# Performance work log

Hardware: AMD Instinct MI355X
Metric: run time of the kernel (lower is better)

## Reference

```python
import jax, jax.numpy as jnp
import numpy as np

N = 16384      # num_nodes (mamba seq_len)
D = 256        # input_dim
HOPS = 3
E = 262144     # num edges
DI = 512       # d_inner = expand*dim
DS = 16        # d_state
DC = 4         # d_conv


def _ln(x, g, b):
    m = jnp.mean(x, -1, keepdims=True)
    v = jnp.var(x, -1, keepdims=True)
    return (x - m) / jnp.sqrt(v + 1e-5) * g + b


def setup_inputs() -> dict:
    key = jax.random.key(0)
    ks = jax.random.split(key, 20)
    g = lambda i, shape, s=0.02: jax.random.normal(ks[i], shape, jnp.float32) * s
    z = lambda *s: jnp.zeros(s, jnp.float32)
    o = lambda *s: jnp.ones(s, jnp.float32)
    return {
        "x": jax.random.normal(ks[0], (HOPS, N, D), jnp.float32),
        "edge_index": jax.random.randint(ks[1], (2, E), 0, N),
        "perm_noise": jax.random.uniform(ks[2], (N,), jnp.float32),
        "hop_w": g(3, (HOPS * D, D)), "hop_b": z(D), "hop_ln_g": o(D), "hop_ln_b": z(D),
        "gat_w": g(4, (D, D)), "gat_att_src": g(5, (D,)), "gat_att_dst": g(6, (D,)), "gat_b": z(D),
        "in_proj_w": g(7, (D, 2 * DI)),
        "conv_w": g(8, (DI, DC), 0.1),
        "x_proj_w": g(9, (DI, DS + 1)),
        "dt_w": g(10, (1, DI)), "dt_b": z(DI),
        "A_log": g(11, (DI, DS)),
        "D_param": o(DI),
        "out_w": g(12, (DI, D)), "out_b": z(D),
        "mlp_w1": g(13, (2 * D, D)), "mlp_b1": z(D), "mlp_ln_g": o(D), "mlp_ln_b": z(D),
        "mlp_w2": g(14, (D, D)), "mlp_b2": z(D),
    }


def _forward(x, edge_index, perm_noise, hop_w, hop_b, hop_ln_g, hop_ln_b,
             gat_w, gat_att_src, gat_att_dst, gat_b, in_proj_w, conv_w,
             x_proj_w, dt_w, dt_b, A_log, D_param, out_w, out_b,
             mlp_w1, mlp_b1, mlp_ln_g, mlp_ln_b, mlp_w2, mlp_b2):
    n = x.shape[1]
    # [hops,N,D] -> [N, hops*D] -> hop_proj
    xf = jnp.transpose(x, (1, 0, 2)).reshape(n, -1)
    xf = jax.nn.silu(_ln(xf @ hop_w + hop_b, hop_ln_g, hop_ln_b))

    # --- GATConv (heads=1, add_self_loops, negative_slope=0.2, eval dropout) ---
    h = xf @ gat_w                                   # [N,D]
    sl = jnp.arange(n)
    src = jnp.concatenate([edge_index[0], sl])
    dst = jnp.concatenate([edge_index[1], sl])
    e = jax.nn.leaky_relu((h @ gat_att_src)[src] + (h @ gat_att_dst)[dst], 0.2)
    emax = jax.ops.segment_max(e, dst, num_segments=n)
    ee = jnp.exp(e - emax[dst])
    denom = jax.ops.segment_sum(ee, dst, num_segments=n)
    alpha = ee / denom[dst]
    x_mpnn = jax.ops.segment_sum(alpha[:, None] * h[src], dst, num_segments=n) + gat_b

    # --- NodeProcessor: degree-based sort with small random noise ---
    deg = jax.ops.segment_sum(jnp.ones((edge_index.shape[1],), jnp.float32),
                              edge_index[0], num_segments=n)
    sorted_idx = jnp.argsort(deg + perm_noise * 0.1)
    u0 = xf[sorted_idx][None]                        # [1,N,D]

    # --- MambaBlock ---
    xz = u0 @ in_proj_w                              # [1,N,2*DI]
    xm, zgate = jnp.split(xz, 2, axis=-1)
    # depthwise causal conv1d (pad d_conv-1 left == torch pad both + slice[:L])
    xm_t = jnp.transpose(xm, (0, 2, 1))              # [1,DI,N]
    xm_t = jax.lax.conv_general_dilated(xm_t, conv_w[:, None, :], (1,),
                                        [(DC - 1, 0)], feature_group_count=DI)
    xm = jax.nn.silu(jnp.transpose(xm_t, (0, 2, 1)))  # [1,N,DI]
    x_dbl = xm @ x_proj_w                            # [1,N,DS+1]
    dt = jax.nn.softplus(x_dbl[..., :1] @ dt_w + dt_b)  # [1,N,DI]
    Bm = x_dbl[..., 1:]                              # [1,N,DS]
    A = -jnp.exp(A_log)                              # [DI,DS]

    def step(hst, inp):
        dti, Bi = inp                                # [1,DI],[1,DS]
        hst = jnp.exp(A * dti[..., None]) * hst + dti[..., None] * Bi[:, None, :]
        return hst, jnp.einsum('bdn,bn->bd', hst, Bi)

    h0 = jnp.zeros((1, DI, DS), xm.dtype)
    _, ys = jax.lax.scan(step, h0, (jnp.transpose(dt, (1, 0, 2)),
                                    jnp.transpose(Bm, (1, 0, 2))))
    y = jnp.transpose(ys, (1, 0, 2)) + xm * D_param  # [1,N,DI]
    y = y * jax.nn.silu(zgate)
    x_mamba = (y @ out_w + out_b)[0]                 # [N,D]

    reverse_idx = jnp.argsort(sorted_idx)
    x_mamba = x_mamba[reverse_idx]

    cat = jnp.concatenate([x_mpnn, x_mamba], axis=-1)
    out = jax.nn.silu(_ln(cat @ mlp_w1 + mlp_b1, mlp_ln_g, mlp_ln_b)) @ mlp_w2 + mlp_b2
    return out  # dim_proj is Identity (input_dim == output_dim)


def reference(x, edge_index, perm_noise, hop_w, hop_b, hop_ln_g, hop_ln_b,
              gat_w, gat_att_src, gat_att_dst, gat_b, in_proj_w, conv_w,
              x_proj_w, dt_w, dt_b, A_log, D_param, out_w, out_b,
              mlp_w1, mlp_b1, mlp_ln_g, mlp_ln_b, mlp_w2, mlp_b2):
    return _forward(x, edge_index, perm_noise, hop_w, hop_b, hop_ln_g, hop_ln_b,
                    gat_w, gat_att_src, gat_att_dst, gat_b, in_proj_w, conv_w,
                    x_proj_w, dt_w, dt_b, A_log, D_param, out_w, out_b,
                    mlp_w1, mlp_b1, mlp_ln_g, mlp_ln_b, mlp_w2, mlp_b2)
```

## Files before the change

### kernel.cpp

```cpp
#include <hip/hip_runtime.h>

#define N_   16384
#define D_   256
#define E_   262144
#define ET_  278528
#define DI_  512
#define CH_  512
#define CL_  32
#define GS_  16
#define NG_  32

typedef __attribute__((ext_vector_type(8))) short short8;
typedef __attribute__((ext_vector_type(4))) float f32x4;
typedef unsigned short ushort_t;

static __device__ __forceinline__ float wave_sum(float v){
#pragma unroll
  for (int m = 1; m < 64; m <<= 1) v += __shfl_xor(v, m);
  return v;
}
static __device__ __forceinline__ float wave_max(float v){
#pragma unroll
  for (int m = 1; m < 64; m <<= 1) v = fmaxf(v, __shfl_xor(v, m));
  return v;
}
static __device__ __forceinline__ float silu_f(float x){ return x / (1.f + __expf(-x)); }
static __device__ __forceinline__ float softplus_f(float v){
  return fmaxf(v, 0.f) + __logf(1.f + __expf(-fabsf(v)));
}
static __device__ __forceinline__ float fexp2(float x){ return __builtin_amdgcn_exp2f(x); }
static __device__ __forceinline__ ushort_t f2b(float f){
  unsigned u = __float_as_uint(f);
  return (ushort_t)((u + 0x7fffu + ((u >> 16) & 1u)) >> 16);
}
static __device__ __forceinline__ float b2f(ushort_t u){
  return __uint_as_float(((unsigned)u) << 16);
}
#define GLDS16(gp, lp) __builtin_amdgcn_global_load_lds( \
    (const __attribute__((address_space(1))) unsigned int*)(gp), \
    (__attribute__((address_space(3))) unsigned int*)(lp), 16, 0, 0)

__global__ __launch_bounds__(256) void marker_kernel(float* __restrict__ out){
  out[threadIdx.x] = 1e9f;
}

__global__ __launch_bounds__(256) void permute_kernel(const float* __restrict__ x, ushort_t* __restrict__ xcat){
  int idx = blockIdx.x * 256 + threadIdx.x;
  if (idx >= 3 * N_ * 64) return;
  int d4  = idx & 63;
  int n   = (idx >> 6) & (N_ - 1);
  int hop = idx >> 20;
  float4 v = ((const float4*)x)[((size_t)hop << 20) + ((size_t)n << 6) + d4];
  ushort4 o; o.x = f2b(v.x); o.y = f2b(v.y); o.z = f2b(v.z); o.w = f2b(v.w);
  ((ushort4*)xcat)[(size_t)n * 192 + hop * 64 + d4] = o;
}

__global__ __launch_bounds__(256) void wconv_kernel(const float* __restrict__ W, int K, int N,
                                                    ushort_t* __restrict__ BT){
  __shared__ float t[32][33];
  const int k0 = blockIdx.x * 32, n0 = blockIdx.y * 32;
  const int tr = threadIdx.x & 31, tc = threadIdx.x >> 5;
#pragma unroll
  for (int r = tc; r < 32; r += 8) {
    int k = k0 + r, n = n0 + tr;
    t[r][tr] = (k < K && n < N) ? W[(size_t)k * N + n] : 0.f;
  }
  __syncthreads();
#pragma unroll
  for (int r = tc; r < 32; r += 8) {
    int n = n0 + r, k = k0 + tr;
    BT[(size_t)n * K + k] = f2b(t[tr][r]);
  }
}

__global__ __launch_bounds__(256) void mgemm_kernel(
    const ushort_t* __restrict__ A, int lda,
    const ushort_t* __restrict__ BT, int ldbt, int N,
    void* __restrict__ C, int ldc, int c_off, int c_bf16,
    const float* __restrict__ bias, const int* __restrict__ row_map, int K)
{
  __shared__ __align__(16) ushort_t Al[64 * 32];
  __shared__ __align__(16) ushort_t Bl[64 * 32];
  const int tid = threadIdx.x;
  const int lane = tid & 63;
  const int wid = tid >> 6;
  const int wr = wid >> 1, wc = wid & 1;
  const int m0 = blockIdx.x * 64, n0 = blockIdx.y * 64;
  const int fr = lane & 15, fq = lane >> 4;
  const int srow = tid >> 2, scg = (tid & 3) << 3;
  f32x4 acc[2][2] = {};
  for (int k0 = 0; k0 < K; k0 += 32) {
    __syncthreads();
    GLDS16(&A [(size_t)(m0 + srow) * lda  + k0 + scg], &Al[(size_t)wid * 512]);
    GLDS16(&BT[(size_t)(n0 + srow) * ldbt + k0 + scg], &Bl[(size_t)wid * 512]);
    __syncthreads();
    short8 af[2], bfr[2];
#pragma unroll
    for (int m = 0; m < 2; ++m) af[m]  = *(const short8*)&Al[(wr * 32 + m * 16 + fr) * 32 + fq * 8];
#pragma unroll
    for (int n = 0; n < 2; ++n) bfr[n] = *(const short8*)&Bl[(wc * 32 + n * 16 + fr) * 32 + fq * 8];
#pragma unroll
    for (int n = 0; n < 2; ++n)
#pragma unroll
      for (int m = 0; m < 2; ++m)
        acc[m][n] = __builtin_amdgcn_mfma_f32_16x16x32_bf16(af[m], bfr[n], acc[m][n], 0, 0, 0);
  }
#pragma unroll
  for (int m = 0; m < 2; ++m)
#pragma unroll
    for (int n = 0; n < 2; ++n) {
      int col = n0 + wc * 32 + n * 16 + fr;
      if (col >= N) continue;
      float bv = bias ? bias[col] : 0.f;
#pragma unroll
      for (int j = 0; j < 4; ++j) {
        int row = m0 + wr * 32 + m * 16 + fq * 4 + j;
        int orow = row_map ? row_map[row] : row;
        float v = acc[m][n][j] + bv;
        if (c_bf16) ((ushort_t*)C)[(size_t)orow * ldc + c_off + col] = f2b(v);
        else        ((float*)C)   [(size_t)orow * ldc + c_off + col] = v;
      }
    }
}

__global__ __launch_bounds__(256) void ln_silu_kernel(const float* __restrict__ x, ushort_t* __restrict__ o8,
                                                      const float* __restrict__ g, const float* __restrict__ b){
  __shared__ float red[4];
  const int row = blockIdx.x; const int t = threadIdx.x;
  float v = x[(size_t)row * 256 + t];
  float sv = wave_sum(v);
  if ((t & 63) == 0) red[t >> 6] = sv;
  __syncthreads();
  float mean = (red[0] + red[1] + red[2] + red[3]) * (1.f / 256.f);
  __syncthreads();
  float dv = v - mean;
  float sq = wave_sum(dv * dv);
  if ((t & 63) == 0) red[t >> 6] = sq;
  __syncthreads();
  float var = (red[0] + red[1] + red[2] + red[3]) * (1.f / 256.f);
  float o = dv * rsqrtf(var + 1e-5f) * g[t] + b[t];
  o8[(size_t)row * 256 + t] = f2b(silu_f(o));
}

__global__ __launch_bounds__(256) void att_scores_kernel(const ushort_t* __restrict__ h, const float* __restrict__ asr,
                                                         const float* __restrict__ adt, float* __restrict__ as_, float* __restrict__ ad_){
  int wid = threadIdx.x >> 6, lane = threadIdx.x & 63;
  int n = blockIdx.x * 4 + wid;
  float s1 = 0.f, s2 = 0.f;
  for (int f = lane; f < 256; f += 64) {
    float hv = b2f(h[(size_t)n * 256 + f]);
    s1 = fmaf(hv, asr[f], s1); s2 = fmaf(hv, adt[f], s2);
  }
  s1 = wave_sum(s1); s2 = wave_sum(s2);
  if (lane == 0) { as_[n] = s1; ad_[n] = s2; }
}

__global__ __launch_bounds__(256) void count_kernel(const int* __restrict__ ei, int* __restrict__ cnt_in, int* __restrict__ deg_out){
  int i = blockIdx.x * 256 + threadIdx.x;
  if (i >= ET_) return;
  int dst = (i < E_) ? ei[E_ + i] : (i - E_);
  atomicAdd(&cnt_in[dst], 1);
  if (i < E_) atomicAdd(&deg_out[ei[i]], 1);
}

__global__ __launch_bounds__(1024) void scan_offsets_kernel(const int* __restrict__ cnt, int* __restrict__ off, int* __restrict__ cursor){
  __shared__ int part[1024];
  int t = threadIdx.x;
  int base = t * 16;
  int local[16]; int s = 0;
#pragma unroll
  for (int i = 0; i < 16; ++i) { local[i] = s; s += cnt[base + i]; }
  part[t] = s; __syncthreads();
  for (int d = 1; d < 1024; d <<= 1) {
    int val = part[t];
    int add = (t >= d) ? part[t - d] : 0;
    __syncthreads();
    part[t] = val + add;
    __syncthreads();
  }
  int prev = (t > 0) ? part[t - 1] : 0;
#pragma unroll
  for (int i = 0; i < 16; ++i) { int o = prev + local[i]; off[base + i] = o; cursor[base + i] = o; }
  if (t == 1023) off[N_] = part[1023];
}

__global__ __launch_bounds__(256) void scatter_kernel(const int* __restrict__ ei, int* __restrict__ cursor, int* __restrict__ csr){
  int i = blockIdx.x * 256 + threadIdx.x;
  if (i >= ET_) return;
  int dst = (i < E_) ? ei[E_ + i] : (i - E_);
  int pos = atomicAdd(&cursor[dst], 1);
  csr[pos] = i;
}

__global__ __launch_bounds__(256) void gat_agg_kernel(const int* __restrict__ ei, const int* __restrict__ off, const int* __restrict__ csr,
                                                      const float* __restrict__ as_, const float* __restrict__ ad_,
                                                      const ushort_t* __restrict__ h, const float* __restrict__ gat_b, ushort_t* __restrict__ cat){
  const int dst = blockIdx.x;
  const int t = threadIdx.x;
  const int o0 = off[dst];
  int deg = off[dst + 1] - o0;
  if (deg > 1024) deg = 1024;
  __shared__ int   ssrc[1024];
  __shared__ float se[1024];
  __shared__ float red[4];
  const float adv = ad_[dst];
  float m = -1e30f;
  for (int j = t; j < deg; j += 256) {
    int eid = csr[o0 + j];
    int src = (eid < E_) ? ei[eid] : (eid - E_);
    float e = as_[src] + adv;
    e = (e >= 0.f) ? e : 0.2f * e;
    ssrc[j] = src; se[j] = e;
    m = fmaxf(m, e);
  }
  m = wave_max(m);
  if ((t & 63) == 0) red[t >> 6] = m;
  __syncthreads();
  m = fmaxf(fmaxf(red[0], red[1]), fmaxf(red[2], red[3]));
  __syncthreads();
  float dsum = 0.f;
  for (int j = t; j < deg; j += 256) { float x = __expf(se[j] - m); se[j] = x; dsum += x; }
  dsum = wave_sum(dsum);
  if ((t & 63) == 0) red[t >> 6] = dsum;
  __syncthreads();
  float inv = 1.f / (red[0] + red[1] + red[2] + red[3]);
  float acc = gat_b[t];
  for (int j = 0; j < deg; ++j) acc = fmaf(se[j] * inv, b2f(h[(size_t)ssrc[j] * 256 + t]), acc);
  cat[(size_t)dst * 512 + t] = f2b(acc);
}

__global__ __launch_bounds__(256) void key_kernel(const int* __restrict__ degO, const float* __restrict__ noise, unsigned long long* __restrict__ keys){
  int n = blockIdx.x * 256 + threadIdx.x;
  if (n >= N_) return;
  float k = __fadd_rn((float)degO[n], __fmul_rn(noise[n], 0.1f));
  unsigned u = __float_as_uint(k);
  u = (u & 0x80000000u) ? ~u : (u | 0x80000000u);
  keys[n] = ((unsigned long long)u << 32) | (unsigned)n;
}

__global__ __launch_bounds__(256) void rank_part_kernel(const unsigned long long* __restrict__ keys, int* __restrict__ rank){
  __shared__ unsigned long long tile[512];
  const int i = blockIdx.x * 256 + threadIdx.x;
  const unsigned long long ki = keys[i];
  const int base = blockIdx.y * 512;
  for (int j = threadIdx.x; j < 512; j += 256) tile[j] = keys[base + j];
  __syncthreads();
  int r = 0;
#pragma unroll 16
  for (int j = 0; j < 512; ++j) r += (tile[j] < ki);
  atomicAdd(&rank[i], r);
}
__global__ __launch_bounds__(256) void rank_scatter_kernel(const int* __restrict__ rank, int* __restrict__ sidx){
  int i = blockIdx.x * 256 + threadIdx.x;
  sidx[rank[i]] = i;
}

__global__ __launch_bounds__(64) void gather_kernel(const ushort_t* __restrict__ xf, const int* __restrict__ sidx, ushort_t* __restrict__ u0){
  int i = blockIdx.x, t = threadIdx.x;
  ((uint2*)u0)[(size_t)i * 64 + t] = ((const uint2*)xf)[(size_t)sidx[i] * 64 + t];
}

__global__ __launch_bounds__(256) void conv_silu_kernel(const float* __restrict__ xz, const float* __restrict__ cw, ushort_t* __restrict__ xm){
  int idx = blockIdx.x * 256 + threadIdx.x;
  if (idx >= N_ * DI_) return;
  int n = idx >> 9, c = idx & 511;
  float acc = 0.f;
#pragma unroll
  for (int k = 0; k < 4; ++k) {
    int nn = n - 3 + k;
    if (nn >= 0) acc = fmaf(xz[(size_t)nn * 1024 + c], cw[c * 4 + k], acc);
  }
  xm[idx] = f2b(silu_f(acc));
}

__global__ __launch_bounds__(256) void scan_p1_kernel(const float* __restrict__ xdbl,
    const float* __restrict__ dt_w, const float* __restrict__ dt_b, const float* __restrict__ A_log,
    float* __restrict__ a_sum, float* __restrict__ b_final)
{
  const int t = threadIdx.x;
  const int d = blockIdx.x * 128 + (t >> 1);
  const int sh = (t & 1) * 8;
  const int c = blockIdx.y;
  float Ac2[8];
#pragma unroll
  for (int k = 0; k < 8; ++k) Ac2[k] = -__expf(A_log[d * 16 + sh + k]) * 1.44269504f;
  const float dwv = dt_w[d], dbv = dt_b[d];
  __shared__ float sx[CL_];
  __shared__ __align__(16) float sB[CL_][16];
  for (int idx = t; idx < CL_ * 17; idx += 256) {
    float v = xdbl[(size_t)c * (CL_ * 17) + idx];
    int row = idx / 17, col = idx - row * 17;
    if (col == 0) sx[row] = v; else sB[row][col - 1] = v;
  }
  __syncthreads();
  float h[8] = {};
  float dts = 0.f;
#pragma unroll 2
  for (int i = 0; i < CL_; ++i) {
    float dtv = softplus_f(fmaf(sx[i], dwv, dbv));
    dts += dtv;
    float4 b0 = *(const float4*)&sB[i][sh];
    float4 b1 = *(const float4*)&sB[i][sh + 4];
    h[0] = fmaf(fexp2(Ac2[0] * dtv), h[0], dtv * b0.x);
    h[1] = fmaf(fexp2(Ac2[1] * dtv), h[1], dtv * b0.y);
    h[2] = fmaf(fexp2(Ac2[2] * dtv), h[2], dtv * b0.z);
    h[3] = fmaf(fexp2(Ac2[3] * dtv), h[3], dtv * b0.w);
    h[4] = fmaf(fexp2(Ac2[4] * dtv), h[4], dtv * b1.x);
    h[5] = fmaf(fexp2(Ac2[5] * dtv), h[5], dtv * b1.y);
    h[6] = fmaf(fexp2(Ac2[6] * dtv), h[6], dtv * b1.z);
    h[7] = fmaf(fexp2(Ac2[7] * dtv), h[7], dtv * b1.w);
  }
  if ((t & 1) == 0) a_sum[c * 512 + d] = dts;
#pragma unroll
  for (int k = 0; k < 8; ++k) b_final[((size_t)c * 16 + sh + k) * 512 + d] = h[k];
}

__global__ __launch_bounds__(256) void scan_mid1_kernel(const float* __restrict__ a_sum,
    const float* __restrict__ b_final, const float* __restrict__ A_log,
    float* __restrict__ ga, float* __restrict__ gb)
{
  const int tid = blockIdx.x * 256 + threadIdx.x;
  const int d = tid & 511;
  const int s = (tid >> 9) & 15;
  const int g = tid >> 13;
  const float Ac = -__expf(A_log[d * 16 + s]);
  const int c0 = g * GS_;
  float ag = 0.f, Bg = 0.f;
  float an = a_sum[c0 * 512 + d];
  float bn = b_final[((size_t)c0 * 16 + s) * 512 + d];
#pragma unroll
  for (int k = 0; k < GS_; ++k) {
    float a = an, b = bn;
    if (k + 1 < GS_) {
      an = a_sum[(c0 + k + 1) * 512 + d];
      bn = b_final[((size_t)(c0 + k + 1) * 16 + s) * 512 + d];
    }
    Bg = fmaf(__expf(Ac * a), Bg, b);
    ag += a;
  }
  gb[((size_t)g * 16 + s) * 512 + d] = Bg;
  if (s == 0) ga[g * 512 + d] = ag;
}

__global__ __launch_bounds__(256) void scan_mid2_kernel(const float* __restrict__ ga,
    const float* __restrict__ gb, const float* __restrict__ A_log, float* __restrict__ ginit)
{
  const int tid = blockIdx.x * 256 + threadIdx.x;
  const int d = tid & 511;
  const int s = tid >> 9;
  const float Ac = -__expf(A_log[d * 16 + s]);
  float gar[NG_], gbr[NG_];
#pragma unroll
  for (int g = 0; g < NG_; ++g) {
    gar[g] = ga[g * 512 + d];
    gbr[g] = gb[((size_t)g * 16 + s) * 512 + d];
  }
  float h = 0.f;
#pragma unroll
  for (int g = 0; g < NG_; ++g) {
    ginit[((size_t)g * 16 + s) * 512 + d] = h;
    h = fmaf(__expf(Ac * gar[g]), h, gbr[g]);
  }
}

__global__ __launch_bounds__(256) void scan_mid3_kernel(const float* __restrict__ a_sum,
    const float* __restrict__ b_final, const float* __restrict__ A_log,
    const float* __restrict__ ginit, float* __restrict__ init)
{
  const int tid = blockIdx.x * 256 + threadIdx.x;
  const int d = tid & 511;
  const int s = (tid >> 9) & 15;
  const int g = tid >> 13;
  const float Ac = -__expf(A_log[d * 16 + s]);
  const int c0 = g * GS_;
  float h = ginit[((size_t)g * 16 + s) * 512 + d];
  float an = a_sum[c0 * 512 + d];
  float bn = b_final[((size_t)c0 * 16 + s) * 512 + d];
#pragma unroll
  for (int k = 0; k < GS_; ++k) {
    float a = an, b = bn;
    if (k + 1 < GS_) {
      an = a_sum[(c0 + k + 1) * 512 + d];
      bn = b_final[((size_t)(c0 + k + 1) * 16 + s) * 512 + d];
    }
    init[((size_t)(c0 + k) * 16 + s) * 512 + d] = h;
    h = fmaf(__expf(Ac * a), h, b);
  }
}

__global__ __launch_bounds__(256) void scan_p3_kernel(const float* __restrict__ xdbl,
    const float* __restrict__ dt_w, const float* __restrict__ dt_b, const float* __restrict__ A_log,
    const float* __restrict__ init, const ushort_t* __restrict__ xm, const float* __restrict__ Dp,
    const float* __restrict__ xz, ushort_t* __restrict__ y_bf)
{
  const int t = threadIdx.x;
  const int d = blockIdx.x * 128 + (t >> 1);
  const int sh = (t & 1) * 8;
  const int c = blockIdx.y;
  float Ac2[8];
#pragma unroll
  for (int k = 0; k < 8; ++k) Ac2[k] = -__expf(A_log[d * 16 + sh + k]) * 1.44269504f;
  const float dwv = dt_w[d], dbv = dt_b[d], dpv = Dp[d];
  __shared__ float sx[CL_];
  __shared__ __align__(16) float sB[CL_][16];
  for (int idx = t; idx < CL_ * 17; idx += 256) {
    float v = xdbl[(size_t)c * (CL_ * 17) + idx];
    int row = idx / 17, col = idx - row * 17;
    if (col == 0) sx[row] = v; else sB[row][col - 1] = v;
  }
  __syncthreads();
  float h[8];
#pragma unroll
  for (int k = 0; k < 8; ++k) h[k] = init[((size_t)c * 16 + sh + k) * 512 + d];
  const int n0 = c * CL_;
  const ushort_t* xmp = xm   + (size_t)n0 * 512  + d;
  const float*    zp  = xz   + (size_t)n0 * 1024 + 512 + d;
  ushort_t*       yp  = y_bf + (size_t)n0 * 512  + d;
#pragma unroll 2
  for (int i = 0; i < CL_; ++i) {
    float dtv = softplus_f(fmaf(sx[i], dwv, dbv));
    float4 b0 = *(const float4*)&sB[i][sh];
    float4 b1 = *(const float4*)&sB[i][sh + 4];
    h[0] = fmaf(fexp2(Ac2[0] * dtv), h[0], dtv * b0.x);
    h[1] = fmaf(fexp2(Ac2[1] * dtv), h[1], dtv * b0.y);
    h[2] = fmaf(fexp2(Ac2[2] * dtv), h[2], dtv * b0.z);
    h[3] = fmaf(fexp2(Ac2[3] * dtv), h[3], dtv * b0.w);
    h[4] = fmaf(fexp2(Ac2[4] * dtv), h[4], dtv * b1.x);
    h[5] = fmaf(fexp2(Ac2[5] * dtv), h[5], dtv * b1.y);
    h[6] = fmaf(fexp2(Ac2[6] * dtv), h[6], dtv * b1.z);
    h[7] = fmaf(fexp2(Ac2[7] * dtv), h[7], dtv * b1.w);
    float y = h[0] * b0.x;
    y = fmaf(h[1], b0.y, y); y = fmaf(h[2], b0.z, y); y = fmaf(h[3], b0.w, y);
    y = fmaf(h[4], b1.x, y); y = fmaf(h[5], b1.y, y); y = fmaf(h[6], b1.z, y);
    y = fmaf(h[7], b1.w, y);
    y += __shfl_xor(y, 1);
    if ((t & 1) == 0) {
      float yv = fmaf(b2f(*xmp), dpv, y);
      float z = *zp;
      *yp = f2b(yv * silu_f(z));
    }
    xmp += 512; zp += 1024; yp += 512;
  }
}

extern "C" void kernel_launch(void* const* d_in, const int* in_sizes, int n_in,
                              void* d_out, int out_size, void* d_ws, size_t ws_size,
                              hipStream_t stream)
{
  (void)in_sizes; (void)n_in; (void)out_size;
  const float* x         = (const float*)d_in[0];
  const int*   ei        = (const int*)d_in[1];
  const float* pnoise    = (const float*)d_in[2];
  const float* hop_w     = (const float*)d_in[3];
  const float* hop_b     = (const float*)d_in[4];
  const float* hop_ln_g  = (const float*)d_in[5];
  const float* hop_ln_b  = (const float*)d_in[6];
  const float* gat_w     = (const float*)d_in[7];
  const float* att_src   = (const float*)d_in[8];
  const float* att_dst   = (const float*)d_in[9];
  const float* gat_b     = (const float*)d_in[10];
  const float* in_proj_w = (const float*)d_in[11];
  const float* conv_w    = (const float*)d_in[12];
  const float* x_proj_w  = (const float*)d_in[13];
  const float* dt_w      = (const float*)d_in[14];
  const float* dt_b      = (const float*)d_in[15];
  const float* A_log     = (const float*)d_in[16];
  const float* D_param   = (const float*)d_in[17];
  const float* out_w     = (const float*)d_in[18];
  const float* out_b     = (const float*)d_in[19];
  const float* mlp_w1    = (const float*)d_in[20];
  const float* mlp_b1    = (const float*)d_in[21];
  const float* mlp_ln_g  = (const float*)d_in[22];
  const float* mlp_ln_b  = (const float*)d_in[23];
  const float* mlp_w2    = (const float*)d_in[24];
  const float* mlp_b2    = (const float*)d_in[25];
  float* out = (float*)d_out;

  char* w = (char*)d_ws;
  auto alloc = [&](size_t bytes) -> void* {
    void* p = (void*)w; w += (bytes + 255) & ~(size_t)255; return p;
  };
  float*    xz     = (float*)alloc((size_t)N_ * 1024 * 4);
  float*    mlp1f  = (float*)alloc((size_t)N_ * 256 * 4);
  ushort_t* xf_bf  = (ushort_t*)alloc((size_t)N_ * 256 * 2);
  ushort_t* h_bf   = (ushort_t*)alloc((size_t)N_ * 256 * 2);
  ushort_t* u0_bf  = (ushort_t*)alloc((size_t)N_ * 256 * 2);
  ushort_t* xm_bf  = (ushort_t*)alloc((size_t)N_ * 512 * 2);
  ushort_t* y_bf   = (ushort_t*)alloc((size_t)N_ * 512 * 2);
  ushort_t* cat_bf = (ushort_t*)alloc((size_t)N_ * 512 * 2);
  ushort_t* m1_bf  = (ushort_t*)alloc((size_t)N_ * 256 * 2);
  float*    xdbl   = (float*)alloc((size_t)N_ * 17 * 4);
  float*    as_    = (float*)alloc((size_t)N_ * 4);
  float*    ad_    = (float*)alloc((size_t)N_ * 4);
  int* cnt    = (int*)alloc((size_t)N_ * 4);
  int* degO   = (int*)alloc((size_t)N_ * 4);
  int* rank   = (int*)alloc((size_t)N_ * 4);
  int* cursor = (int*)alloc((size_t)N_ * 4);
  int* off    = (int*)alloc((size_t)(N_ + 1) * 4);
  int* sidx   = (int*)alloc((size_t)N_ * 4);
  int* csr    = (int*)alloc((size_t)ET_ * 4);
  unsigned long long* keys = (unsigned long long*)alloc((size_t)N_ * 8);
  float* ga    = (float*)alloc((size_t)NG_ * 512 * 4);
  float* gb    = (float*)alloc((size_t)NG_ * 16 * 512 * 4);
  float* ginit = (float*)alloc((size_t)NG_ * 16 * 512 * 4);
  ushort_t* bt_hop = (ushort_t*)alloc((size_t)256 * 768 * 2);
  ushort_t* bt_gat = (ushort_t*)alloc((size_t)256 * 256 * 2);
  ushort_t* bt_inp = (ushort_t*)alloc((size_t)1024 * 256 * 2);
  ushort_t* bt_xp  = (ushort_t*)alloc((size_t)128 * 512 * 2);
  ushort_t* bt_out = (ushort_t*)alloc((size_t)256 * 512 * 2);
  ushort_t* bt_m1  = (ushort_t*)alloc((size_t)256 * 512 * 2);
  ushort_t* bt_m2  = (ushort_t*)alloc((size_t)256 * 256 * 2);
  ushort_t* xcat_bf = (ushort_t*)xz;
  float*    b_final = mlp1f;
  float*    init    = (float*)xf_bf;
  float*    a_sum   = (float*)csr;
  size_t needed = (size_t)(w - (char*)d_ws);
  if (needed > ws_size) {
    marker_kernel<<<1, 256, 0, stream>>>(out);
    return;
  }

  hipMemsetAsync(cnt, 0, 3 * (size_t)N_ * 4, stream);

  wconv_kernel<<<dim3(24, 8),  256, 0, stream>>>(hop_w,     768, 256,  bt_hop);
  wconv_kernel<<<dim3(8, 8),   256, 0, stream>>>(gat_w,     256, 256,  bt_gat);
  wconv_kernel<<<dim3(8, 32),  256, 0, stream>>>(in_proj_w, 256, 1024, bt_inp);
  wconv_kernel<<<dim3(16, 4),  256, 0, stream>>>(x_proj_w,  512, 17,   bt_xp);
  wconv_kernel<<<dim3(16, 8),  256, 0, stream>>>(out_w,     512, 256,  bt_out);
  wconv_kernel<<<dim3(16, 8),  256, 0, stream>>>(mlp_w1,    512, 256,  bt_m1);
  wconv_kernel<<<dim3(8, 8),   256, 0, stream>>>(mlp_w2,    256, 256,  bt_m2);

  permute_kernel<<<(3 * N_ * 64) / 256, 256, 0, stream>>>(x, xcat_bf);
  mgemm_kernel<<<dim3(256, 4), 256, 0, stream>>>(xcat_bf, 768, bt_hop, 768, 256, mlp1f, 256, 0, 0, hop_b, nullptr, 768);
  ln_silu_kernel<<<N_, 256, 0, stream>>>(mlp1f, xf_bf, hop_ln_g, hop_ln_b);
  mgemm_kernel<<<dim3(256, 4), 256, 0, stream>>>(xf_bf, 256, bt_gat, 256, 256, h_bf, 256, 0, 1, nullptr, nullptr, 256);
  att_scores_kernel<<<N_ / 4, 256, 0, stream>>>(h_bf, att_src, att_dst, as_, ad_);
  count_kernel<<<(ET_ + 255) / 256, 256, 0, stream>>>(ei, cnt, degO);
  scan_offsets_kernel<<<1, 1024, 0, stream>>>(cnt, off, cursor);
  scatter_kernel<<<(ET_ + 255) / 256, 256, 0, stream>>>(ei, cursor, csr);
  gat_agg_kernel<<<N_, 256, 0, stream>>>(ei, off, csr, as_, ad_, h_bf, gat_b, cat_bf);
  key_kernel<<<N_ / 256, 256, 0, stream>>>(degO, pnoise, keys);
  rank_part_kernel<<<dim3(N_ / 256, 32), 256, 0, stream>>>(keys, rank);
  rank_scatter_kernel<<<N_ / 256, 256, 0, stream>>>(rank, sidx);
  gather_kernel<<<N_, 64, 0, stream>>>(xf_bf, sidx, u0_bf);
  mgemm_kernel<<<dim3(256, 16), 256, 0, stream>>>(u0_bf, 256, bt_inp, 256, 1024, xz, 1024, 0, 0, nullptr, nullptr, 256);
  conv_silu_kernel<<<(N_ * DI_) / 256, 256, 0, stream>>>(xz, conv_w, xm_bf);
  mgemm_kernel<<<dim3(256, 1), 256, 0, stream>>>(xm_bf, 512, bt_xp, 512, 17, xdbl, 17, 0, 0, nullptr, nullptr, 512);
  scan_p1_kernel<<<dim3(4, CH_), 256, 0, stream>>>(xdbl, dt_w, dt_b, A_log, a_sum, b_final);
  scan_mid1_kernel<<<(NG_ * 16 * 512) / 256, 256, 0, stream>>>(a_sum, b_final, A_log, ga, gb);
  scan_mid2_kernel<<<32, 256, 0, stream>>>(ga, gb, A_log, ginit);
  scan_mid3_kernel<<<(NG_ * 16 * 512) / 256, 256, 0, stream>>>(a_sum, b_final, A_log, ginit, init);
  scan_p3_kernel<<<dim3(4, CH_), 256, 0, stream>>>(xdbl, dt_w, dt_b, A_log, init, xm_bf, D_param, xz, y_bf);
  mgemm_kernel<<<dim3(256, 4), 256, 0, stream>>>(y_bf, 512, bt_out, 512, 256, cat_bf, 512, 256, 1, out_b, sidx, 512);
  mgemm_kernel<<<dim3(256, 4), 256, 0, stream>>>(cat_bf, 512, bt_m1, 512, 256, mlp1f, 256, 0, 0, mlp_b1, nullptr, 512);
  ln_silu_kernel<<<N_, 256, 0, stream>>>(mlp1f, m1_bf, mlp_ln_g, mlp_ln_b);
  mgemm_kernel<<<dim3(256, 4), 256, 0, stream>>>(m1_bf, 256, bt_m2, 256, 256, out, 256, 0, 0, mlp_b2, nullptr, 256);
}
```

Measured before the change: 409.8 us.

## Store in_proj output as bf16 and give each scan thread all 16 states

```diff
diff --git a/kernel.cpp b/kernel.cpp
--- a/kernel.cpp
+++ b/kernel.cpp
@@ -260,17 +260,22 @@
   ((uint2*)u0)[(size_t)i * 64 + t] = ((const uint2*)xf)[(size_t)sidx[i] * 64 + t];
 }
 
-__global__ __launch_bounds__(256) void conv_silu_kernel(const float* __restrict__ xz, const float* __restrict__ cw, ushort_t* __restrict__ xm){
+__global__ __launch_bounds__(256) void conv_silu_kernel(const ushort_t* __restrict__ xz, const float* __restrict__ cw, ushort_t* __restrict__ xm){
   int idx = blockIdx.x * 256 + threadIdx.x;
-  if (idx >= N_ * DI_) return;
-  int n = idx >> 9, c = idx & 511;
-  float acc = 0.f;
+  if (idx >= N_ * 256) return;
+  int n = idx >> 8, cp = (idx & 255) << 1;
+  float acc0 = 0.f, acc1 = 0.f;
 #pragma unroll
   for (int k = 0; k < 4; ++k) {
     int nn = n - 3 + k;
-    if (nn >= 0) acc = fmaf(xz[(size_t)nn * 1024 + c], cw[c * 4 + k], acc);
-  }
-  xm[idx] = f2b(silu_f(acc));
+    if (nn >= 0) {
+      unsigned u = *(const unsigned*)&xz[(size_t)nn * 1024 + cp];
+      acc0 = fmaf(b2f((ushort_t)(u & 0xffffu)), cw[cp * 4 + k], acc0);
+      acc1 = fmaf(b2f((ushort_t)(u >> 16)),     cw[(cp + 1) * 4 + k], acc1);
+    }
+  }
+  unsigned o = (unsigned)f2b(silu_f(acc0)) | ((unsigned)f2b(silu_f(acc1)) << 16);
+  *(unsigned*)&xm[(size_t)n * 512 + cp] = o;
 }
 
 __global__ __launch_bounds__(256) void scan_p1_kernel(const float* __restrict__ xdbl,
@@ -278,12 +283,11 @@
     float* __restrict__ a_sum, float* __restrict__ b_final)
 {
   const int t = threadIdx.x;
-  const int d = blockIdx.x * 128 + (t >> 1);
-  const int sh = (t & 1) * 8;
+  const int d = blockIdx.x * 256 + t;
   const int c = blockIdx.y;
-  float Ac2[8];
-#pragma unroll
-  for (int k = 0; k < 8; ++k) Ac2[k] = -__expf(A_log[d * 16 + sh + k]) * 1.44269504f;
+  float Ac2[16];
+#pragma unroll
+  for (int k = 0; k < 16; ++k) Ac2[k] = -__expf(A_log[d * 16 + k]) * 1.44269504f;
   const float dwv = dt_w[d], dbv = dt_b[d];
   __shared__ float sx[CL_];
   __shared__ __align__(16) float sB[CL_][16];
@@ -293,26 +297,35 @@
     if (col == 0) sx[row] = v; else sB[row][col - 1] = v;
   }
   __syncthreads();
-  float h[8] = {};
+  float h[16] = {};
   float dts = 0.f;
-#pragma unroll 2
   for (int i = 0; i < CL_; ++i) {
     float dtv = softplus_f(fmaf(sx[i], dwv, dbv));
     dts += dtv;
-    float4 b0 = *(const float4*)&sB[i][sh];
-    float4 b1 = *(const float4*)&sB[i][sh + 4];
-    h[0] = fmaf(fexp2(Ac2[0] * dtv), h[0], dtv * b0.x);
-    h[1] = fmaf(fexp2(Ac2[1] * dtv), h[1], dtv * b0.y);
-    h[2] = fmaf(fexp2(Ac2[2] * dtv), h[2], dtv * b0.z);
-    h[3] = fmaf(fexp2(Ac2[3] * dtv), h[3], dtv * b0.w);
-    h[4] = fmaf(fexp2(Ac2[4] * dtv), h[4], dtv * b1.x);
-    h[5] = fmaf(fexp2(Ac2[5] * dtv), h[5], dtv * b1.y);
-    h[6] = fmaf(fexp2(Ac2[6] * dtv), h[6], dtv * b1.z);
-    h[7] = fmaf(fexp2(Ac2[7] * dtv), h[7], dtv * b1.w);
-  }
-  if ((t & 1) == 0) a_sum[c * 512 + d] = dts;
-#pragma unroll
-  for (int k = 0; k < 8; ++k) b_final[((size_t)c * 16 + sh + k) * 512 + d] = h[k];
+    float4 b0 = *(const float4*)&sB[i][0];
+    float4 b1 = *(const float4*)&sB[i][4];
+    float4 b2 = *(const float4*)&sB[i][8];
+    float4 b3 = *(const float4*)&sB[i][12];
+    h[0]  = fmaf(fexp2(Ac2[0]  * dtv), h[0],  dtv * b0.x);
+    h[1]  = fmaf(fexp2(Ac2[1]  * dtv), h[1],  dtv * b0.y);
+    h[2]  = fmaf(fexp2(Ac2[2]  * dtv), h[2],  dtv * b0.z);
+    h[3]  = fmaf(fexp2(Ac2[3]  * dtv), h[3],  dtv * b0.w);
+    h[4]  = fmaf(fexp2(Ac2[4]  * dtv), h[4],  dtv * b1.x);
+    h[5]  = fmaf(fexp2(Ac2[5]  * dtv), h[5],  dtv * b1.y);
+    h[6]  = fmaf(fexp2(Ac2[6]  * dtv), h[6],  dtv * b1.z);
+    h[7]  = fmaf(fexp2(Ac2[7]  * dtv), h[7],  dtv * b1.w);
+    h[8]  = fmaf(fexp2(Ac2[8]  * dtv), h[8],  dtv * b2.x);
+    h[9]  = fmaf(fexp2(Ac2[9]  * dtv), h[9],  dtv * b2.y);
+    h[10] = fmaf(fexp2(Ac2[10] * dtv), h[10], dtv * b2.z);
+    h[11] = fmaf(fexp2(Ac2[11] * dtv), h[11], dtv * b2.w);
+    h[12] = fmaf(fexp2(Ac2[12] * dtv), h[12], dtv * b3.x);
+    h[13] = fmaf(fexp2(Ac2[13] * dtv), h[13], dtv * b3.y);
+    h[14] = fmaf(fexp2(Ac2[14] * dtv), h[14], dtv * b3.z);
+    h[15] = fmaf(fexp2(Ac2[15] * dtv), h[15], dtv * b3.w);
+  }
+  a_sum[c * 512 + d] = dts;
+#pragma unroll
+  for (int k = 0; k < 16; ++k) b_final[((size_t)c * 16 + k) * 512 + d] = h[k];
 }
 
 __global__ __launch_bounds__(256) void scan_mid1_kernel(const float* __restrict__ a_sum,
@@ -391,15 +404,14 @@
 __global__ __launch_bounds__(256) void scan_p3_kernel(const float* __restrict__ xdbl,
     const float* __restrict__ dt_w, const float* __restrict__ dt_b, const float* __restrict__ A_log,
     const float* __restrict__ init, const ushort_t* __restrict__ xm, const float* __restrict__ Dp,
-    const float* __restrict__ xz, ushort_t* __restrict__ y_bf)
+    const ushort_t* __restrict__ xz, ushort_t* __restrict__ y_bf)
 {
   const int t = threadIdx.x;
-  const int d = blockIdx.x * 128 + (t >> 1);
-  const int sh = (t & 1) * 8;
+  const int d = blockIdx.x * 256 + t;
   const int c = blockIdx.y;
-  float Ac2[8];
-#pragma unroll
-  for (int k = 0; k < 8; ++k) Ac2[k] = -__expf(A_log[d * 16 + sh + k]) * 1.44269504f;
+  float Ac2[16];
+#pragma unroll
+  for (int k = 0; k < 16; ++k) Ac2[k] = -__expf(A_log[d * 16 + k]) * 1.44269504f;
   const float dwv = dt_w[d], dbv = dt_b[d], dpv = Dp[d];
   __shared__ float sx[CL_];
   __shared__ __align__(16) float sB[CL_][16];
@@ -409,36 +421,44 @@
     if (col == 0) sx[row] = v; else sB[row][col - 1] = v;
   }
   __syncthreads();
-  float h[8];
-#pragma unroll
-  for (int k = 0; k < 8; ++k) h[k] = init[((size_t)c * 16 + sh + k) * 512 + d];
+  float h[16];
+#pragma unroll
+  for (int k = 0; k < 16; ++k) h[k] = init[((size_t)c * 16 + k) * 512 + d];
   const int n0 = c * CL_;
   const ushort_t* xmp = xm   + (size_t)n0 * 512  + d;
-  const float*    zp  = xz   + (size_t)n0 * 1024 + 512 + d;
+  const ushort_t* zp  = xz   + (size_t)n0 * 1024 + 512 + d;
   ushort_t*       yp  = y_bf + (size_t)n0 * 512  + d;
-#pragma unroll 2
   for (int i = 0; i < CL_; ++i) {
     float dtv = softplus_f(fmaf(sx[i], dwv, dbv));
-    float4 b0 = *(const float4*)&sB[i][sh];
-    float4 b1 = *(const float4*)&sB[i][sh + 4];
-    h[0] = fmaf(fexp2(Ac2[0] * dtv), h[0], dtv * b0.x);
-    h[1] = fmaf(fexp2(Ac2[1] * dtv), h[1], dtv * b0.y);
-    h[2] = fmaf(fexp2(Ac2[2] * dtv), h[2], dtv * b0.z);
-    h[3] = fmaf(fexp2(Ac2[3] * dtv), h[3], dtv * b0.w);
-    h[4] = fmaf(fexp2(Ac2[4] * dtv), h[4], dtv * b1.x);
-    h[5] = fmaf(fexp2(Ac2[5] * dtv), h[5], dtv * b1.y);
-    h[6] = fmaf(fexp2(Ac2[6] * dtv), h[6], dtv * b1.z);
-    h[7] = fmaf(fexp2(Ac2[7] * dtv), h[7], dtv * b1.w);
+    float4 b0 = *(const float4*)&sB[i][0];
+    float4 b1 = *(const float4*)&sB[i][4];
+    float4 b2 = *(const float4*)&sB[i][8];
+    float4 b3 = *(const float4*)&sB[i][12];
+    h[0]  = fmaf(fexp2(Ac2[0]  * dtv), h[0],  dtv * b0.x);
+    h[1]  = fmaf(fexp2(Ac2[1]  * dtv), h[1],  dtv * b0.y);
+    h[2]  = fmaf(fexp2(Ac2[2]  * dtv), h[2],  dtv * b0.z);
+    h[3]  = fmaf(fexp2(Ac2[3]  * dtv), h[3],  dtv * b0.w);
+    h[4]  = fmaf(fexp2(Ac2[4]  * dtv), h[4],  dtv * b1.x);
+    h[5]  = fmaf(fexp2(Ac2[5]  * dtv), h[5],  dtv * b1.y);
+    h[6]  = fmaf(fexp2(Ac2[6]  * dtv), h[6],  dtv * b1.z);
+    h[7]  = fmaf(fexp2(Ac2[7]  * dtv), h[7],  dtv * b1.w);
+    h[8]  = fmaf(fexp2(Ac2[8]  * dtv), h[8],  dtv * b2.x);
+    h[9]  = fmaf(fexp2(Ac2[9]  * dtv), h[9],  dtv * b2.y);
+    h[10] = fmaf(fexp2(Ac2[10] * dtv), h[10], dtv * b2.z);
+    h[11] = fmaf(fexp2(Ac2[11] * dtv), h[11], dtv * b2.w);
+    h[12] = fmaf(fexp2(Ac2[12] * dtv), h[12], dtv * b3.x);
+    h[13] = fmaf(fexp2(Ac2[13] * dtv), h[13], dtv * b3.y);
+    h[14] = fmaf(fexp2(Ac2[14] * dtv), h[14], dtv * b3.z);
+    h[15] = fmaf(fexp2(Ac2[15] * dtv), h[15], dtv * b3.w);
     float y = h[0] * b0.x;
-    y = fmaf(h[1], b0.y, y); y = fmaf(h[2], b0.z, y); y = fmaf(h[3], b0.w, y);
-    y = fmaf(h[4], b1.x, y); y = fmaf(h[5], b1.y, y); y = fmaf(h[6], b1.z, y);
-    y = fmaf(h[7], b1.w, y);
-    y += __shfl_xor(y, 1);
-    if ((t & 1) == 0) {
-      float yv = fmaf(b2f(*xmp), dpv, y);
-      float z = *zp;
-      *yp = f2b(yv * silu_f(z));
-    }
+    y = fmaf(h[1],  b0.y, y); y = fmaf(h[2],  b0.z, y); y = fmaf(h[3],  b0.w, y);
+    y = fmaf(h[4],  b1.x, y); y = fmaf(h[5],  b1.y, y); y = fmaf(h[6],  b1.z, y);
+    y = fmaf(h[7],  b1.w, y); y = fmaf(h[8],  b2.x, y); y = fmaf(h[9],  b2.y, y);
+    y = fmaf(h[10], b2.z, y); y = fmaf(h[11], b2.w, y); y = fmaf(h[12], b3.x, y);
+    y = fmaf(h[13], b3.y, y); y = fmaf(h[14], b3.z, y); y = fmaf(h[15], b3.w, y);
+    float yv = fmaf(b2f(*xmp), dpv, y);
+    float z = b2f(*zp);
+    *yp = f2b(yv * silu_f(z));
     xmp += 512; zp += 1024; yp += 512;
   }
 }
@@ -480,7 +500,7 @@
   auto alloc = [&](size_t bytes) -> void* {
     void* p = (void*)w; w += (bytes + 255) & ~(size_t)255; return p;
   };
-  float*    xz     = (float*)alloc((size_t)N_ * 1024 * 4);
+  ushort_t* xz_bf  = (ushort_t*)alloc((size_t)N_ * 1024 * 2);
   float*    mlp1f  = (float*)alloc((size_t)N_ * 256 * 4);
   ushort_t* xf_bf  = (ushort_t*)alloc((size_t)N_ * 256 * 2);
   ushort_t* h_bf   = (ushort_t*)alloc((size_t)N_ * 256 * 2);
@@ -510,7 +530,7 @@
   ushort_t* bt_out = (ushort_t*)alloc((size_t)256 * 512 * 2);
   ushort_t* bt_m1  = (ushort_t*)alloc((size_t)256 * 512 * 2);
   ushort_t* bt_m2  = (ushort_t*)alloc((size_t)256 * 256 * 2);
-  ushort_t* xcat_bf = (ushort_t*)xz;
+  ushort_t* xcat_bf = xz_bf;
   float*    b_final = mlp1f;
   float*    init    = (float*)xf_bf;
   float*    a_sum   = (float*)csr;
@@ -543,14 +563,14 @@
   rank_part_kernel<<<dim3(N_ / 256, 32), 256, 0, stream>>>(keys, rank);
   rank_scatter_kernel<<<N_ / 256, 256, 0, stream>>>(rank, sidx);
   gather_kernel<<<N_, 64, 0, stream>>>(xf_bf, sidx, u0_bf);
-  mgemm_kernel<<<dim3(256, 16), 256, 0, stream>>>(u0_bf, 256, bt_inp, 256, 1024, xz, 1024, 0, 0, nullptr, nullptr, 256);
-  conv_silu_kernel<<<(N_ * DI_) / 256, 256, 0, stream>>>(xz, conv_w, xm_bf);
+  mgemm_kernel<<<dim3(256, 16), 256, 0, stream>>>(u0_bf, 256, bt_inp, 256, 1024, xz_bf, 1024, 0, 1, nullptr, nullptr, 256);
+  conv_silu_kernel<<<(N_ * 256) / 256, 256, 0, stream>>>(xz_bf, conv_w, xm_bf);
   mgemm_kernel<<<dim3(256, 1), 256, 0, stream>>>(xm_bf, 512, bt_xp, 512, 17, xdbl, 17, 0, 0, nullptr, nullptr, 512);
-  scan_p1_kernel<<<dim3(4, CH_), 256, 0, stream>>>(xdbl, dt_w, dt_b, A_log, a_sum, b_final);
+  scan_p1_kernel<<<dim3(2, CH_), 256, 0, stream>>>(xdbl, dt_w, dt_b, A_log, a_sum, b_final);
   scan_mid1_kernel<<<(NG_ * 16 * 512) / 256, 256, 0, stream>>>(a_sum, b_final, A_log, ga, gb);
   scan_mid2_kernel<<<32, 256, 0, stream>>>(ga, gb, A_log, ginit);
   scan_mid3_kernel<<<(NG_ * 16 * 512) / 256, 256, 0, stream>>>(a_sum, b_final, A_log, ginit, init);
-  scan_p3_kernel<<<dim3(4, CH_), 256, 0, stream>>>(xdbl, dt_w, dt_b, A_log, init, xm_bf, D_param, xz, y_bf);
+  scan_p3_kernel<<<dim3(2, CH_), 256, 0, stream>>>(xdbl, dt_w, dt_b, A_log, init, xm_bf, D_param, xz_bf, y_bf);
   mgemm_kernel<<<dim3(256, 4), 256, 0, stream>>>(y_bf, 512, bt_out, 512, 256, cat_bf, 512, 256, 1, out_b, sidx, 512);
   mgemm_kernel<<<dim3(256, 4), 256, 0, stream>>>(cat_bf, 512, bt_m1, 512, 256, mlp1f, 256, 0, 0, mlp_b1, nullptr, 512);
   ln_silu_kernel<<<N_, 256, 0, stream>>>(mlp1f, m1_bf, mlp_ln_g, mlp_ln_b);
```

Measured after the change: 418.2 us. +2.0%, slower.
